# Optimization experiments

Hardware: AMD Instinct MI355X
Metric: run time of the kernel (lower is better)

## Reference

```python
import jax, jax.numpy as jnp
import numpy as np

# ---- constants mirroring the module config ----
TIMESTEPS = 1000
N_GT = 3            # GT phases {stable, pre-shock, shock}
NUM_EXPERTS = 6     # 2 sub-experts per GT phase; phase L -> experts {L, L+3}
LAMBDA_REG = 0.01
LAMBDA_LB = 0.01
PHASE_WEIGHTS = np.array([1.0, 5.0, 5.0], dtype=np.float32)


def _sinusoidal_embed(t, dim):
    # standard DDPM sinusoidal timestep embedding -> [B, dim]
    half = dim // 2
    freqs = jnp.exp(-jnp.log(10000.0) * jnp.arange(half, dtype=jnp.float32) / half)
    args = t.astype(jnp.float32)[:, None] * freqs[None, :]
    return jnp.concatenate([jnp.sin(args), jnp.cos(args)], axis=-1)


def _alphas_bar():
    betas = jnp.linspace(1e-4, 0.02, TIMESTEPS, dtype=jnp.float32)
    return jnp.cumprod(1.0 - betas)


def setup_inputs() -> dict:
    B, Tp, Tf, Df, Ds, dm, E, H = 512, 256, 64, 64, 32, 512, NUM_EXPERTS, 512
    key = jax.random.key(0)
    ks = jax.random.split(key, 16)
    s = 0.02  # init scale
    d_in = Df + 2 * dm  # noisy features + global ctx + t embedding
    return {
        'observed_data': jax.random.normal(ks[0], (B, Tp, Df), jnp.float32),
        'future_data':   jax.random.normal(ks[1], (B, Tf, Df), jnp.float32),
        'static_context': jax.random.normal(ks[2], (B, Ds), jnp.float32),
        'eps':           jax.random.normal(ks[3], (B, Tf, Df), jnp.float32),
        'phase_label':   jax.random.randint(ks[4], (B,), 0, N_GT),
        't':             jax.random.randint(ks[5], (B,), 0, TIMESTEPS),
        'W_enc':    jax.random.normal(ks[6], (Df, dm), jnp.float32) * s,
        'b_enc':    jnp.zeros((dm,), jnp.float32),
        'W_stat':   jax.random.normal(ks[7], (Ds, dm), jnp.float32) * s,
        'W_router': jax.random.normal(ks[8], (dm, E), jnp.float32) * s,
        'b_router': jnp.zeros((E,), jnp.float32),
        'W1': jax.random.normal(ks[9],  (E, d_in, H), jnp.float32) * s,
        'b1': jnp.zeros((E, H), jnp.float32),
        'W2': jax.random.normal(ks[10], (E, H, Df), jnp.float32) * s,
        'b2': jnp.zeros((E, Df), jnp.float32),
    }


def reference(observed_data, future_data, static_context, eps,
              W_enc, b_enc, W_stat, W_router, b_router,
              W1, b1, W2, b2, phase_label, t):
    B, Tf, Df = future_data.shape
    E = W1.shape[0]
    dm = W_enc.shape[1]

    # ---- frozen encoder (torch.no_grad in the original) ----
    ctx_seq = jax.nn.gelu(observed_data @ W_enc + (static_context @ W_stat)[:, None, :] + b_enc)  # [B,Tp,dm]
    global_ctx = ctx_seq.mean(axis=1)                                                             # [B,dm]
    ctx_seq = jax.lax.stop_gradient(ctx_seq)
    global_ctx = jax.lax.stop_gradient(global_ctx)

    # ---- router (trainable) ----
    router_logits = global_ctx @ W_router + b_router        # [B,E]
    router_probs = jax.nn.softmax(router_logits, axis=-1)

    # ---- GT-masked top-1 routing: phase p -> argmax over experts {p, p+3} ----
    selected = jnp.zeros((B,), jnp.int32)
    for p in range(N_GT):
        sub = jnp.stack([router_probs[:, p], router_probs[:, p + N_GT]], axis=1)  # [B,2]
        winner = p + N_GT * jnp.argmax(sub, axis=1).astype(jnp.int32)
        selected = jnp.where(phase_label == p, winner, selected)

    # ---- diffusion scheduler: add_noise ----
    ab = _alphas_bar()[t]                                   # [B]
    noisy_fut = (jnp.sqrt(ab)[:, None, None] * future_data
                 + jnp.sqrt(1.0 - ab)[:, None, None] * eps)  # [B,Tf,Df]

    # ---- expert backbones: run all E experts densely, then gather routed output ----
    t_emb = _sinusoidal_embed(t, dm)                        # [B,dm]
    cond = jnp.concatenate([
        noisy_fut,
        jnp.broadcast_to(global_ctx[:, None, :], (B, Tf, dm)),
        jnp.broadcast_to(t_emb[:, None, :],      (B, Tf, dm)),
    ], axis=-1)                                             # [B,Tf,Din]
    h = jax.nn.gelu(jnp.einsum('btd,edh->ebth', cond, W1) + b1[:, None, None, :])
    outputs_all = jnp.einsum('ebth,ehf->ebtf', h, W2) + b2[:, None, None, :]  # [E,B,Tf,Df]

    pred = outputs_all[selected, jnp.arange(B)]             # [B,Tf,Df] gradient-surgery dispatch
    loss_raw = jnp.mean((pred - eps) ** 2, axis=(1, 2))     # per-sample MSE, [B]

    # weighted_loss * count/B summed over experts == mean(loss_raw * w[selected%3])
    lw = jnp.asarray(PHASE_WEIGHTS)
    w_sample = lw[selected % N_GT]
    total_loss = jnp.mean(loss_raw * w_sample)

    # ---- consistency regularization on a fixed 4-sample subset ----
    S = min(B, 4)
    out_sub = outputs_all[:, :S]                            # [E,S,Tf,Df]
    chain = jnp.float32(0.0)
    for i in [0, 1, 3, 4]:
        if i + 1 < E:
            chain += jnp.mean((out_sub[i] - out_sub[i + 1]) ** 2)
    for i in range(N_GT):
        if i + N_GT < E:
            chain += jnp.mean((out_sub[i] - out_sub[i + N_GT]) ** 2)
    diff = out_sub[:, :, 1:] - out_sub[:, :, :-1]
    smooth = jnp.sum(jnp.mean(diff ** 2, axis=(1, 2, 3)))
    total_loss += (chain + 0.5 * smooth) * LAMBDA_REG

    # ---- load-balance loss ----
    onehot = (selected[:, None] == jnp.arange(E)[None, :]).astype(jnp.float32)  # [B,E]
    f = onehot.mean(axis=0)
    P = router_probs.mean(axis=0)
    total_loss += LAMBDA_LB * E * jnp.sum(f * P)

    return total_loss
```

## Files before the change

kernel.cpp:

```cpp
#include <hip/hip_runtime.h>

typedef float  f32x4 __attribute__((ext_vector_type(4)));
typedef short  s16x8 __attribute__((ext_vector_type(8)));
typedef unsigned short u16;
typedef u16    u16x4 __attribute__((ext_vector_type(4)));

#define TIMESTEPS 1000

#define WS_ALPHAS   0
#define WS_FREQS    1024
#define WS_PROBS    1536
#define WS_SELECTED 4608
#define WS_LOSSB    5632
#define WS_FLAG1    6144
#define WS_PARTS    7680
#define WS_FLAG     7700
#define WS_P0       8192
#define WS_XC       270336
#define WS_HSTAT    532480
#define WS_HSTAT2   794624
#define WS_OUTSUB   806912
#define WS_BIAS     2691072
#define WS_U16BYTE  3620864
#define U_WENCT     0
#define U_W1T       32768
#define U_W2T       3375104

__device__ __forceinline__ u16 f2bf(float x){
    unsigned u = __builtin_bit_cast(unsigned, x);
    unsigned r = (u + 0x7FFFu + ((u >> 16) & 1u)) >> 16;
    return (u16)r;
}

__device__ __forceinline__ float gelu_f(float x){
    float x2 = x * x;
    float t  = x * fmaf(0.035677408136f, x2, 0.7978845608028654f);
    float ex = __builtin_amdgcn_exp2f(t * 2.885390081777927f);
    float r  = __builtin_amdgcn_rcpf(ex + 1.0f);
    return fmaf(-x, r, x);
}

__device__ __forceinline__ void mfma16(f32x4& c, s16x8 a, s16x8 b){
    asm volatile("v_mfma_f32_16x16x32_bf16 %0, %1, %2, %0" : "+v"(c) : "v"(a), "v"(b));
}

__global__ __launch_bounds__(256) void k0(const float* __restrict__ Wenc,
        const float* __restrict__ W1, const float* __restrict__ W2,
        const float* __restrict__ stat, const float* __restrict__ Wstat,
        const float* __restrict__ benc, u16* __restrict__ uws, float* __restrict__ ws){
    __shared__ float sT[64][65];
    float* sp = &sT[0][0];
    int bid = blockIdx.x, tid = threadIdx.x;
    if(bid == 0){
        ws[WS_FREQS + tid] = expf(-logf(10000.0f) * (float)tid / 256.0f);
        float p = 1.f;
        #pragma unroll
        for(int r = 0; r < 4; r++){
            int i = tid*4 + r;
            if(i < TIMESTEPS){
                float beta = 0.0001f + (0.02f - 0.0001f) * ((float)i / 999.0f);
                p *= (1.0f - beta);
            }
        }
        sp[tid] = p;
        __syncthreads();
        for(int st = 1; st < 256; st <<= 1){
            float v = (tid >= st) ? sp[tid - st] : 1.0f;
            __syncthreads();
            sp[tid] *= v;
            __syncthreads();
        }
        float run = (tid == 0) ? 1.0f : sp[tid - 1];
        for(int r = 0; r < 4; r++){
            int i = tid*4 + r;
            if(i < TIMESTEPS){
                float beta = 0.0001f + (0.02f - 0.0001f) * ((float)i / 999.0f);
                run *= (1.0f - beta);
                ws[WS_ALPHAS + i] = run;
            }
        }
        return;
    }
    if(bid <= 8){
        int jt = bid - 1;
        int r = tid >> 2, c0 = (tid & 3) * 16;
        #pragma unroll
        for(int i = 0; i < 4; i++)
            *(f32x4*)&sT[r][c0 + i*4] = *(const f32x4*)&Wenc[(size_t)r*512 + jt*64 + c0 + i*4];
        __syncthreads();
        u16* dst = uws + U_WENCT + (size_t)(jt*64 + r)*64;
        #pragma unroll
        for(int i = 0; i < 4; i++){
            u16x4 pk;
            pk.x = f2bf(sT[c0 + i*4 + 0][r]); pk.y = f2bf(sT[c0 + i*4 + 1][r]);
            pk.z = f2bf(sT[c0 + i*4 + 2][r]); pk.w = f2bf(sT[c0 + i*4 + 3][r]);
            *(u16x4*)&dst[c0 + i*4] = pk;
        }
        return;
    }
    if(bid <= 72){
        float* sSt = sp;
        int g = bid - 9, b0 = g*8;
        sSt[tid] = stat[b0*32 + tid];
        __syncthreads();
        #pragma unroll
        for(int half = 0; half < 2; half++){
            int j = tid + half*256;
            float acc[8] = {0,0,0,0,0,0,0,0};
            for(int s = 0; s < 32; s++){
                float wv = Wstat[s*512 + j];
                #pragma unroll
                for(int bb = 0; bb < 8; bb++) acc[bb] += sSt[bb*32 + s] * wv;
            }
            float bz = benc[j];
            #pragma unroll
            for(int bb = 0; bb < 8; bb++)
                ws[WS_BIAS + (b0 + bb)*512 + j] = acc[bb] + bz;
        }
        return;
    }
    int t = bid - 73;
    const float* src; u16* dst; int K, J, kt, jt;
    if(t < 816){
        int e = t / 136, r = t % 136; kt = r >> 3; jt = r & 7;
        src = W1 + (size_t)e*1088*512; dst = uws + U_W1T + (size_t)e*512*1088; K = 1088; J = 512;
    } else {
        int t2 = t - 816; int e = t2 >> 3; kt = t2 & 7; jt = 0;
        src = W2 + (size_t)e*512*64; dst = uws + U_W2T + (size_t)e*64*512; K = 512; J = 64;
    }
    int r = tid >> 2, c0 = (tid & 3) * 16;
    #pragma unroll
    for(int i = 0; i < 4; i++)
        *(f32x4*)&sT[r][c0 + i*4] = *(const f32x4*)&src[(size_t)(kt*64 + r)*J + jt*64 + c0 + i*4];
    __syncthreads();
    u16* d2 = dst + (size_t)(jt*64 + r)*K + kt*64;
    #pragma unroll
    for(int i = 0; i < 4; i++){
        u16x4 pk;
        pk.x = f2bf(sT[c0 + i*4 + 0][r]); pk.y = f2bf(sT[c0 + i*4 + 1][r]);
        pk.z = f2bf(sT[c0 + i*4 + 2][r]); pk.w = f2bf(sT[c0 + i*4 + 3][r]);
        *(u16x4*)&d2[c0 + i*4] = pk;
    }
}

#define PADX 72
__global__ __launch_bounds__(1024) void k1_enc(const float* __restrict__ obs,
        const u16* __restrict__ uws, const float* __restrict__ Wr,
        const float* __restrict__ br, const int* __restrict__ phase,
        const int* __restrict__ t_arr, float* __restrict__ ws){
    __shared__ u16  sX[256 * PADX];
    __shared__ float sBias[512];
    __shared__ float sG[512];
    __shared__ float sRed[8][6];
    int b = blockIdx.x, tid = threadIdx.x;
    {
        int row = tid >> 2, c0 = (tid & 3) * 16;
        const f32x4* src = (const f32x4*)&obs[((size_t)b*256 + row)*64 + c0];
        u16* dst = &sX[row*PADX + c0];
        #pragma unroll
        for(int i = 0; i < 4; i++){
            f32x4 v = src[i];
            u16x4 pk; pk.x = f2bf(v.x); pk.y = f2bf(v.y); pk.z = f2bf(v.z); pk.w = f2bf(v.w);
            *(u16x4*)(dst + i*4) = pk;
        }
    }
    if(tid < 512) sBias[tid] = ws[WS_BIAS + b*512 + tid];
    __syncthreads();
    int w = tid >> 6, l = tid & 63, lr = l & 15, lk = (l >> 4) * 8;
    const u16* wencT = uws + U_WENCT;
    s16x8 bf[2][2];
    float bias[2];
    #pragma unroll
    for(int n = 0; n < 2; n++){
        int col = w*32 + n*16 + lr;
        bf[n][0] = *(const s16x8*)&wencT[col*64 + lk];
        bf[n][1] = *(const s16x8*)&wencT[col*64 + 32 + lk];
        bias[n]  = sBias[col];
    }
    float cac[2] = {0.f, 0.f};
    for(int mt = 0; mt < 16; mt++){
        s16x8 a0 = *(const s16x8*)&sX[(mt*16 + lr)*PADX + lk];
        s16x8 a1 = *(const s16x8*)&sX[(mt*16 + lr)*PADX + 32 + lk];
        #pragma unroll
        for(int n = 0; n < 2; n++){
            f32x4 acc = {bias[n], bias[n], bias[n], bias[n]};
            mfma16(acc, a0, bf[n][0]);
            mfma16(acc, a1, bf[n][1]);
            cac[n] += gelu_f(acc.x) + gelu_f(acc.y) + gelu_f(acc.z) + gelu_f(acc.w);
        }
    }
    #pragma unroll
    for(int n = 0; n < 2; n++){
        cac[n] += __shfl_xor(cac[n], 16);
        cac[n] += __shfl_xor(cac[n], 32);
    }
    if(l < 16){
        #pragma unroll
        for(int n = 0; n < 2; n++)
            sG[w*32 + n*16 + l] = cac[n] * (1.0f/256.0f);
    }
    __syncthreads();
    if(tid < 512){
        float gv = sG[tid];
        u16* XC = (u16*)(ws + WS_XC);
        XC[b*1024 + tid] = f2bf(gv);
        int tv = t_arr[b];
        float fr = ws[WS_FREQS + (tid & 255)];
        float ang = (float)tv * fr;
        XC[b*1024 + 512 + tid] = f2bf((tid < 256) ? sinf(ang) : cosf(ang));
        float p6[6];
        #pragma unroll
        for(int e = 0; e < 6; e++) p6[e] = gv * Wr[tid*6 + e];
        #pragma unroll
        for(int off = 32; off > 0; off >>= 1)
            #pragma unroll
            for(int e = 0; e < 6; e++) p6[e] += __shfl_down(p6[e], off);
        if(l == 0)
            #pragma unroll
            for(int e = 0; e < 6; e++) sRed[w][e] = p6[e];
    }
    __syncthreads();
    if(tid == 0){
        float logit[6], mx = -1e30f;
        #pragma unroll
        for(int e = 0; e < 6; e++){
            float s = 0.f;
            #pragma unroll
            for(int q = 0; q < 8; q++) s += sRed[q][e];
            logit[e] = s + br[e];
            mx = fmaxf(mx, logit[e]);
        }
        float s = 0.f, p[6];
        #pragma unroll
        for(int e = 0; e < 6; e++){ p[e] = expf(logit[e] - mx); s += p[e]; }
        float inv = 1.0f / s;
        #pragma unroll
        for(int e = 0; e < 6; e++) ws[WS_PROBS + b*6 + e] = p[e] * inv;
        int ph = phase[b];
        int sel = ph + ((logit[ph + 3] > logit[ph]) ? 3 : 0);
        ((int*)ws)[WS_SELECTED + b] = sel;
    }
}

__global__ __launch_bounds__(256) void k3_hstat(const u16* __restrict__ uws,
        const float* __restrict__ b1, float* __restrict__ ws){
    __shared__ int sSrc[64], sDst[64];
    __shared__ int sCnt[8][6], sBase[8][6], sSec[6], sTot[6];
    __shared__ int sChunk[16][3];
    __shared__ int sNch;
    int bid = blockIdx.x, tid = threadIdx.x;
    int w = tid >> 6, l = tid & 63;
    int* wsi = (int*)ws;
    if(bid == 0 && tid == 0) wsi[WS_FLAG] = 0;
    int sv0 = wsi[WS_SELECTED + tid];
    int sv1 = wsi[WS_SELECTED + 256 + tid];
    unsigned long long mym0 = 0, mym1 = 0;
    #pragma unroll
    for(int e = 0; e < 6; e++){
        unsigned long long m0 = __ballot(sv0 == e);
        unsigned long long m1 = __ballot(sv1 == e);
        if(l == 0){ sCnt[w][e] = __popcll(m0); sCnt[4 + w][e] = __popcll(m1); }
        if(sv0 == e) mym0 = m0;
        if(sv1 == e) mym1 = m1;
    }
    if(tid < 64){ sSrc[tid] = 0; sDst[tid] = -1; }
    __syncthreads();
    if(tid == 0){
        int o = 0;
        for(int e = 0; e < 6; e++){
            sSec[e] = o; int t0 = 0;
            for(int g = 0; g < 8; g++){ sBase[g][e] = o; o += sCnt[g][e]; t0 += sCnt[g][e]; }
            sTot[e] = t0; o += 4;
        }
        int nch = 0;
        for(int e = 0; e < 6; e++){
            int len = sTot[e] + 4, st = sSec[e];
            for(int s = 0; s < len; s += 64){
                sChunk[nch][0] = e; sChunk[nch][1] = st + s;
                sChunk[nch][2] = (len - s < 64) ? (len - s) : 64; nch++;
            }
        }
        sNch = nch;
    }
    __syncthreads();
    int c = bid >> 3, jt = bid & 7;
    if(c >= sNch) return;
    int e     = sChunk[c][0];
    int start = sChunk[c][1];
    int len   = sChunk[c][2];
    {
        int rank = __popcll(mym0 & ((1ull << l) - 1ull));
        int pos = sBase[w][sv0] + rank - start;
        if(pos >= 0 && pos < len){ sSrc[pos] = tid; sDst[pos] = WS_HSTAT + tid*512; }
    }
    {
        int rank = __popcll(mym1 & ((1ull << l) - 1ull));
        int pos = sBase[4 + w][sv1] + rank - start;
        if(pos >= 0 && pos < len){ sSrc[pos] = 256 + tid; sDst[pos] = WS_HSTAT + (256 + tid)*512; }
    }
    if(tid < 24){
        int ea = tid >> 2, ba = tid & 3;
        int pos = sSec[ea] + sTot[ea] + ba - start;
        if(pos >= 0 && pos < len){ sSrc[pos] = ba; sDst[pos] = WS_HSTAT2 + (ea*4 + ba)*512; }
    }
    __syncthreads();
    int lr = l & 15, lk = (l >> 4) * 8;
    int col = jt*64 + w*16 + lr;
    const u16* XC = (const u16*)(ws + WS_XC);
    const u16* rowA[4];
    #pragma unroll
    for(int mt = 0; mt < 4; mt++)
        rowA[mt] = XC + (size_t)sSrc[mt*16 + lr]*1024 + lk;
    const u16* bp = uws + U_W1T + ((size_t)e*512 + col)*1088 + 64 + lk;
    f32x4 acc[4];
    {
        float bv = b1[e*512 + col];
        f32x4 z = {bv, bv, bv, bv};
        #pragma unroll
        for(int mt = 0; mt < 4; mt++) acc[mt] = z;
    }
    #pragma unroll 4
    for(int ks = 0; ks < 32; ks++){
        s16x8 bb = *(const s16x8*)(bp + ks*32);
        s16x8 a0 = *(const s16x8*)(rowA[0] + ks*32);
        s16x8 a1 = *(const s16x8*)(rowA[1] + ks*32);
        s16x8 a2 = *(const s16x8*)(rowA[2] + ks*32);
        s16x8 a3 = *(const s16x8*)(rowA[3] + ks*32);
        mfma16(acc[0], a0, bb);
        mfma16(acc[1], a1, bb);
        mfma16(acc[2], a2, bb);
        mfma16(acc[3], a3, bb);
    }
    #pragma unroll
    for(int mt = 0; mt < 4; mt++){
        #pragma unroll
        for(int rg = 0; rg < 4; rg++){
            int r = mt*16 + (l >> 4)*4 + rg;
            int d = sDst[r];
            if(d >= 0) ws[d + col] = acc[mt][rg];
        }
    }
}

#define PADN 72
#define PADH 520
__global__ __launch_bounds__(512) void k4_ffn(const float* __restrict__ fut,
        const float* __restrict__ eps, const int* __restrict__ t_arr,
        const u16* __restrict__ uws, const float* __restrict__ b2,
        float* __restrict__ ws){
    __shared__ u16 sN[64 * PADN];
    __shared__ u16 sH[64 * PADH];
    __shared__ float sHs[512];
    __shared__ float sRed[8];
    int tid = threadIdx.x, bid = blockIdx.x;
    int* wsi = (int*)ws;
    int b, e, store;
    if(bid < 24){ e = bid >> 2; b = bid & 3; store = 1; }
    else { b = bid - 24; e = wsi[WS_SELECTED + b]; store = 0; }
    sHs[tid] = store ? ws[WS_HSTAT2 + (e*4 + b)*512 + tid] : ws[WS_HSTAT + b*512 + tid];
    int tv = t_arr[b];
    float ab = ws[WS_ALPHAS + tv];
    float sa = sqrtf(ab), sb = sqrtf(1.0f - ab);
    {
        int r = tid >> 3, c0 = (tid & 7) * 8;
        const f32x4* pf = (const f32x4*)&fut[((size_t)b*64 + r)*64 + c0];
        const f32x4* pe = (const f32x4*)&eps[((size_t)b*64 + r)*64 + c0];
        f32x4 f0 = pf[0], f1 = pf[1], e0 = pe[0], e1 = pe[1];
        u16x4 p0, p1;
        p0.x = f2bf(sa*f0.x + sb*e0.x); p0.y = f2bf(sa*f0.y + sb*e0.y);
        p0.z = f2bf(sa*f0.z + sb*e0.z); p0.w = f2bf(sa*f0.w + sb*e0.w);
        p1.x = f2bf(sa*f1.x + sb*e1.x); p1.y = f2bf(sa*f1.y + sb*e1.y);
        p1.z = f2bf(sa*f1.z + sb*e1.z); p1.w = f2bf(sa*f1.w + sb*e1.w);
        *(u16x4*)&sN[r*PADN + c0]     = p0;
        *(u16x4*)&sN[r*PADN + c0 + 4] = p1;
    }
    __syncthreads();
    int w = tid >> 6, l = tid & 63, lr = l & 15, lk = (l >> 4) * 8;
    const u16* w1T = uws + U_W1T;
    const u16* w2T = uws + U_W2T;
    s16x8 aw[4][2];
    #pragma unroll
    for(int mt = 0; mt < 4; mt++){
        int jrow = w*64 + mt*16 + lr;
        aw[mt][0] = *(const s16x8*)&w1T[((size_t)e*512 + jrow)*1088 + lk];
        aw[mt][1] = *(const s16x8*)&w1T[((size_t)e*512 + jrow)*1088 + 32 + lk];
    }
    #pragma unroll
    for(int nt = 0; nt < 4; nt++){
        s16x8 nb0 = *(const s16x8*)&sN[(nt*16 + lr)*PADN + lk];
        s16x8 nb1 = *(const s16x8*)&sN[(nt*16 + lr)*PADN + 32 + lk];
        #pragma unroll
        for(int mt = 0; mt < 4; mt++){
            int j0 = w*64 + mt*16 + (l >> 4)*4;
            f32x4 acc = *(const f32x4*)&sHs[j0];
            mfma16(acc, aw[mt][0], nb0);
            mfma16(acc, aw[mt][1], nb1);
            u16x4 pk;
            pk.x = f2bf(gelu_f(acc.x)); pk.y = f2bf(gelu_f(acc.y));
            pk.z = f2bf(gelu_f(acc.z)); pk.w = f2bf(gelu_f(acc.w));
            *(u16x4*)&sH[(nt*16 + lr)*PADH + j0] = pk;
        }
    }
    __syncthreads();
    int mtg = (w >> 2) << 1;
    int nt  = w & 3;
    f32x4 oacc[2];
    {
        float bz = b2[e*64 + nt*16 + lr];
        f32x4 z = {bz, bz, bz, bz}; oacc[0] = z; oacc[1] = z;
    }
    for(int ks = 0; ks < 16; ks++){
        s16x8 bb = *(const s16x8*)&w2T[((size_t)e*64 + nt*16 + lr)*512 + ks*32 + lk];
        #pragma unroll
        for(int i = 0; i < 2; i++){
            s16x8 a = *(const s16x8*)&sH[((mtg + i)*16 + lr)*PADH + ks*32 + lk];
            mfma16(oacc[i], a, bb);
        }
    }
    if(store){
        #pragma unroll
        for(int i = 0; i < 2; i++)
            #pragma unroll
            for(int rg = 0; rg < 4; rg++){
                int row = (mtg + i)*16 + (l >> 4)*4 + rg;
                int col = nt*16 + lr;
                ws[WS_OUTSUB + (e*4 + b)*4096 + row*64 + col] = oacc[i][rg];
            }
    } else {
        float ls = 0.f;
        #pragma unroll
        for(int i = 0; i < 2; i++)
            #pragma unroll
            for(int rg = 0; rg < 4; rg++){
                int row = (mtg + i)*16 + (l >> 4)*4 + rg;
                int col = nt*16 + lr;
                float d = oacc[i][rg] - eps[((size_t)b*64 + row)*64 + col];
                ls += d*d;
            }
        #pragma unroll
        for(int off = 32; off > 0; off >>= 1) ls += __shfl_down(ls, off);
        if(l == 0) sRed[w] = ls;
        __syncthreads();
        if(tid == 0){
            float s = 0.f;
            #pragma unroll
            for(int q = 0; q < 8; q++) s += sRed[q];
            const float pw[3] = {1.f, 5.f, 5.f};
            ws[WS_LOSSB + b] = (s * (1.0f/4096.0f)) * pw[e % 3];
        }
    }
}

__global__ __launch_bounds__(256) void k5_final(float* __restrict__ ws, float* __restrict__ out){
    int bid = blockIdx.x, tid = threadIdx.x;
    int* wsi = (int*)ws;
    if(bid < 13){
        __shared__ float red[256];
        float s = 0.f;
        if(bid < 7){
            const int pa[7] = {0,1,3,4,0,1,2};
            const int pb[7] = {1,2,4,5,3,4,5};
            const float* A  = &ws[WS_OUTSUB + pa[bid]*16384];
            const float* Bp = &ws[WS_OUTSUB + pb[bid]*16384];
            for(int i = tid; i < 4096; i += 256){
                f32x4 a = *(const f32x4*)&A[i*4];
                f32x4 c = *(const f32x4*)&Bp[i*4];
                f32x4 d = a - c;
                s += d.x*d.x + d.y*d.y + d.z*d.z + d.w*d.w;
            }
            s *= (1.0f/16384.0f);
        } else {
            int e = bid - 7;
            const float* O = &ws[WS_OUTSUB + e*16384];
            for(int i = tid; i < 4*63*16; i += 256){
                int sm = i / (63*16); int r = i % (63*16);
                int tf = r / 16; int f4 = (r % 16) * 4;
                f32x4 a = *(const f32x4*)&O[(sm*64 + tf + 1)*64 + f4];
                f32x4 c = *(const f32x4*)&O[(sm*64 + tf)*64 + f4];
                f32x4 d = a - c;
                s += d.x*d.x + d.y*d.y + d.z*d.z + d.w*d.w;
            }
            s *= (1.0f/16128.0f) * 0.5f;
        }
        red[tid] = s;
        __syncthreads();
        for(int st = 128; st > 0; st >>= 1){
            if(tid < st) red[tid] += red[tid + st];
            __syncthreads();
        }
        if(tid == 0){
            ws[WS_PARTS + bid] = red[0];
            __threadfence();
            atomicAdd(&wsi[WS_FLAG], 1);
        }
        return;
    }
    if(tid == 0){
        while(atomicAdd(&wsi[WS_FLAG], 0) < 13) __builtin_amdgcn_s_sleep(2);
    }
    __syncthreads();
    __threadfence();
    __shared__ float sW[4];
    __shared__ float sF[4][6], sP[4][6];
    int w = tid >> 6, l = tid & 63;
    int sel0 = wsi[WS_SELECTED + tid];
    int sel1 = wsi[WS_SELECTED + 256 + tid];
    float lv = ws[WS_LOSSB + tid] + ws[WS_LOSSB + 256 + tid];
    float pv[6], cf[6];
    #pragma unroll
    for(int e = 0; e < 6; e++){
        pv[e] = ws[WS_PROBS + tid*6 + e] + ws[WS_PROBS + (256 + tid)*6 + e];
        cf[e] = ((sel0 == e) ? 1.f : 0.f) + ((sel1 == e) ? 1.f : 0.f);
    }
    #pragma unroll
    for(int off = 32; off > 0; off >>= 1){
        lv += __shfl_down(lv, off);
        #pragma unroll
        for(int e = 0; e < 6; e++){
            pv[e] += __shfl_down(pv[e], off);
            cf[e] += __shfl_down(cf[e], off);
        }
    }
    if(l == 0){
        sW[w] = lv;
        #pragma unroll
        for(int e = 0; e < 6; e++){ sF[w][e] = cf[e]; sP[w][e] = pv[e]; }
    }
    __syncthreads();
    if(tid == 0){
        float total = 0.f;
        for(int q = 0; q < 4; q++) total += sW[q];
        total *= (1.0f/512.0f);
        volatile float* vp = ws + WS_PARTS;
        float reg = 0.f;
        for(int p = 0; p < 13; p++) reg += vp[p];
        total += 0.01f * reg;
        float lb = 0.f;
        for(int e = 0; e < 6; e++){
            float f = 0.f, pp = 0.f;
            for(int q = 0; q < 4; q++){ f += sF[q][e]; pp += sP[q][e]; }
            lb += (f * (1.0f/512.f)) * (pp * (1.0f/512.f));
        }
        out[0] = total + 0.01f * 6.0f * lb;
    }
}

extern "C" void kernel_launch(void* const* d_in, const int* in_sizes, int n_in,
                              void* d_out, int out_size, void* d_ws, size_t ws_size,
                              hipStream_t stream){
    const float* obs  = (const float*)d_in[0];
    const float* fut  = (const float*)d_in[1];
    const float* stat = (const float*)d_in[2];
    const float* eps  = (const float*)d_in[3];
    const int*   phase= (const int*)d_in[4];
    const int*   t    = (const int*)d_in[5];
    const float* Wenc = (const float*)d_in[6];
    const float* benc = (const float*)d_in[7];
    const float* Wstat= (const float*)d_in[8];
    const float* Wr   = (const float*)d_in[9];
    const float* br   = (const float*)d_in[10];
    const float* W1   = (const float*)d_in[11];
    const float* b1   = (const float*)d_in[12];
    const float* W2   = (const float*)d_in[13];
    const float* b2   = (const float*)d_in[14];
    float* ws  = (float*)d_ws;
    u16*   uws = (u16*)((char*)d_ws + WS_U16BYTE);
    float* out = (float*)d_out;

    k0<<<937, 256, 0, stream>>>(Wenc, W1, W2, stat, Wstat, benc, uws, ws);
    k1_enc<<<512, 1024, 0, stream>>>(obs, uws, Wr, br, phase, t, ws);
    k3_hstat<<<112, 256, 0, stream>>>(uws, b1, ws);
    k4_ffn<<<536, 512, 0, stream>>>(fut, eps, t, uws, b2, ws);
    k5_final<<<14, 256, 0, stream>>>(ws, out);
}
```

Measured before the change: 102.5 us.

## Split hidden-stat GEMM along K and FFN along time rows for more blocks

k3_hstat now splits its K reduction into two halves, so it launches twice as many blocks and writes two partial buffers. k4_ffn sums those partials and handles half of the 64 time rows per block, using 256-thread blocks and twice the grid. The consistency-regularisation reduction in k5_final is spread over four times as many blocks, and the per-sample loss weighting moves into the final reduction. The aim is better occupancy of the many CUs on this small-batch workload. The cost is extra partial-sum traffic, W1 slices being reloaded for each time half, and a new workspace buffer placed at the same offset as WS_BIAS.

```diff
diff --git a/kernel.cpp b/kernel.cpp
--- a/kernel.cpp
+++ b/kernel.cpp
@@ -12,15 +12,15 @@
 #define WS_PROBS    1536
 #define WS_SELECTED 4608
 #define WS_LOSSB    5632
-#define WS_FLAG1    6144
 #define WS_PARTS    7680
-#define WS_FLAG     7700
-#define WS_P0       8192
+#define WS_FLAG     7744
+#define WS_HSTATB   8192
 #define WS_XC       270336
 #define WS_HSTAT    532480
 #define WS_HSTAT2   794624
 #define WS_OUTSUB   806912
 #define WS_BIAS     2691072
+#define WS_HSTAT2B  2691072
 #define WS_U16BYTE  3620864
 #define U_WENCT     0
 #define U_W1T       32768
@@ -252,6 +252,7 @@
     int w = tid >> 6, l = tid & 63;
     int* wsi = (int*)ws;
     if(bid == 0 && tid == 0) wsi[WS_FLAG] = 0;
+    int kh = bid & 1, jt = (bid >> 1) & 7, c = bid >> 4;
     int sv0 = wsi[WS_SELECTED + tid];
     int sv1 = wsi[WS_SELECTED + 256 + tid];
     unsigned long long mym0 = 0, mym1 = 0;
@@ -283,25 +284,26 @@
         sNch = nch;
     }
     __syncthreads();
-    int c = bid >> 3, jt = bid & 7;
     if(c >= sNch) return;
     int e     = sChunk[c][0];
     int start = sChunk[c][1];
     int len   = sChunk[c][2];
+    int hstatD  = kh ? WS_HSTATB  : WS_HSTAT;
+    int hstat2D = kh ? WS_HSTAT2B : WS_HSTAT2;
     {
         int rank = __popcll(mym0 & ((1ull << l) - 1ull));
         int pos = sBase[w][sv0] + rank - start;
-        if(pos >= 0 && pos < len){ sSrc[pos] = tid; sDst[pos] = WS_HSTAT + tid*512; }
+        if(pos >= 0 && pos < len){ sSrc[pos] = tid; sDst[pos] = hstatD + tid*512; }
     }
     {
         int rank = __popcll(mym1 & ((1ull << l) - 1ull));
         int pos = sBase[4 + w][sv1] + rank - start;
-        if(pos >= 0 && pos < len){ sSrc[pos] = 256 + tid; sDst[pos] = WS_HSTAT + (256 + tid)*512; }
+        if(pos >= 0 && pos < len){ sSrc[pos] = 256 + tid; sDst[pos] = hstatD + (256 + tid)*512; }
     }
     if(tid < 24){
         int ea = tid >> 2, ba = tid & 3;
         int pos = sSec[ea] + sTot[ea] + ba - start;
-        if(pos >= 0 && pos < len){ sSrc[pos] = ba; sDst[pos] = WS_HSTAT2 + (ea*4 + ba)*512; }
+        if(pos >= 0 && pos < len){ sSrc[pos] = ba; sDst[pos] = hstat2D + (ea*4 + ba)*512; }
     }
     __syncthreads();
     int lr = l & 15, lk = (l >> 4) * 8;
@@ -310,17 +312,17 @@
     const u16* rowA[4];
     #pragma unroll
     for(int mt = 0; mt < 4; mt++)
-        rowA[mt] = XC + (size_t)sSrc[mt*16 + lr]*1024 + lk;
-    const u16* bp = uws + U_W1T + ((size_t)e*512 + col)*1088 + 64 + lk;
+        rowA[mt] = XC + (size_t)sSrc[mt*16 + lr]*1024 + kh*512 + lk;
+    const u16* bp = uws + U_W1T + ((size_t)e*512 + col)*1088 + 64 + kh*512 + lk;
     f32x4 acc[4];
     {
-        float bv = b1[e*512 + col];
+        float bv = kh ? 0.f : b1[e*512 + col];
         f32x4 z = {bv, bv, bv, bv};
         #pragma unroll
         for(int mt = 0; mt < 4; mt++) acc[mt] = z;
     }
     #pragma unroll 4
-    for(int ks = 0; ks < 32; ks++){
+    for(int ks = 0; ks < 16; ks++){
         s16x8 bb = *(const s16x8*)(bp + ks*32);
         s16x8 a0 = *(const s16x8*)(rowA[0] + ks*32);
         s16x8 a1 = *(const s16x8*)(rowA[1] + ks*32);
@@ -344,27 +346,35 @@
 
 #define PADN 72
 #define PADH 520
-__global__ __launch_bounds__(512) void k4_ffn(const float* __restrict__ fut,
+__global__ __launch_bounds__(256) void k4_ffn(const float* __restrict__ fut,
         const float* __restrict__ eps, const int* __restrict__ t_arr,
         const u16* __restrict__ uws, const float* __restrict__ b2,
         float* __restrict__ ws){
-    __shared__ u16 sN[64 * PADN];
-    __shared__ u16 sH[64 * PADH];
+    __shared__ u16 sN[32 * PADN];
+    __shared__ u16 sH[32 * PADH];
     __shared__ float sHs[512];
-    __shared__ float sRed[8];
+    __shared__ float sRed[4];
     int tid = threadIdx.x, bid = blockIdx.x;
     int* wsi = (int*)ws;
-    int b, e, store;
-    if(bid < 24){ e = bid >> 2; b = bid & 3; store = 1; }
-    else { b = bid - 24; e = wsi[WS_SELECTED + b]; store = 0; }
-    sHs[tid] = store ? ws[WS_HSTAT2 + (e*4 + b)*512 + tid] : ws[WS_HSTAT + b*512 + tid];
+    int b, e, store, half;
+    if(bid < 48){ int idx = bid >> 1; half = bid & 1; e = idx >> 2; b = idx & 3; store = 1; }
+    else { int r = bid - 48; b = r >> 1; half = r & 1; e = wsi[WS_SELECTED + b]; store = 0; }
+    int tf0 = half * 32;
+    if(store){
+        int i2 = (e*4 + b)*512;
+        sHs[tid]       = ws[WS_HSTAT2 + i2 + tid]       + ws[WS_HSTAT2B + i2 + tid];
+        sHs[tid + 256] = ws[WS_HSTAT2 + i2 + tid + 256] + ws[WS_HSTAT2B + i2 + tid + 256];
+    } else {
+        sHs[tid]       = ws[WS_HSTAT + b*512 + tid]       + ws[WS_HSTATB + b*512 + tid];
+        sHs[tid + 256] = ws[WS_HSTAT + b*512 + tid + 256] + ws[WS_HSTATB + b*512 + tid + 256];
+    }
     int tv = t_arr[b];
     float ab = ws[WS_ALPHAS + tv];
     float sa = sqrtf(ab), sb = sqrtf(1.0f - ab);
     {
         int r = tid >> 3, c0 = (tid & 7) * 8;
-        const f32x4* pf = (const f32x4*)&fut[((size_t)b*64 + r)*64 + c0];
-        const f32x4* pe = (const f32x4*)&eps[((size_t)b*64 + r)*64 + c0];
+        const f32x4* pf = (const f32x4*)&fut[((size_t)b*64 + tf0 + r)*64 + c0];
+        const f32x4* pe = (const f32x4*)&eps[((size_t)b*64 + tf0 + r)*64 + c0];
         f32x4 f0 = pf[0], f1 = pf[1], e0 = pe[0], e1 = pe[1];
         u16x4 p0, p1;
         p0.x = f2bf(sa*f0.x + sb*e0.x); p0.y = f2bf(sa*f0.y + sb*e0.y);
@@ -378,23 +388,24 @@
     int w = tid >> 6, l = tid & 63, lr = l & 15, lk = (l >> 4) * 8;
     const u16* w1T = uws + U_W1T;
     const u16* w2T = uws + U_W2T;
-    s16x8 aw[4][2];
-    #pragma unroll
-    for(int mt = 0; mt < 4; mt++){
-        int jrow = w*64 + mt*16 + lr;
-        aw[mt][0] = *(const s16x8*)&w1T[((size_t)e*512 + jrow)*1088 + lk];
-        aw[mt][1] = *(const s16x8*)&w1T[((size_t)e*512 + jrow)*1088 + 32 + lk];
-    }
-    #pragma unroll
-    for(int nt = 0; nt < 4; nt++){
-        s16x8 nb0 = *(const s16x8*)&sN[(nt*16 + lr)*PADN + lk];
-        s16x8 nb1 = *(const s16x8*)&sN[(nt*16 + lr)*PADN + 32 + lk];
-        #pragma unroll
-        for(int mt = 0; mt < 4; mt++){
-            int j0 = w*64 + mt*16 + (l >> 4)*4;
-            f32x4 acc = *(const f32x4*)&sHs[j0];
-            mfma16(acc, aw[mt][0], nb0);
-            mfma16(acc, aw[mt][1], nb1);
+    s16x8 nb[2][2];
+    #pragma unroll
+    for(int nt = 0; nt < 2; nt++){
+        nb[nt][0] = *(const s16x8*)&sN[(nt*16 + lr)*PADN + lk];
+        nb[nt][1] = *(const s16x8*)&sN[(nt*16 + lr)*PADN + 32 + lk];
+    }
+    #pragma unroll
+    for(int mt = 0; mt < 8; mt++){
+        int jrow = w*128 + mt*16 + lr;
+        s16x8 aw0 = *(const s16x8*)&w1T[((size_t)e*512 + jrow)*1088 + lk];
+        s16x8 aw1 = *(const s16x8*)&w1T[((size_t)e*512 + jrow)*1088 + 32 + lk];
+        int j0 = w*128 + mt*16 + (l >> 4)*4;
+        f32x4 hsv = *(const f32x4*)&sHs[j0];
+        #pragma unroll
+        for(int nt = 0; nt < 2; nt++){
+            f32x4 acc = hsv;
+            mfma16(acc, aw0, nb[nt][0]);
+            mfma16(acc, aw1, nb[nt][1]);
             u16x4 pk;
             pk.x = f2bf(gelu_f(acc.x)); pk.y = f2bf(gelu_f(acc.y));
             pk.z = f2bf(gelu_f(acc.z)); pk.w = f2bf(gelu_f(acc.w));
@@ -402,18 +413,17 @@
         }
     }
     __syncthreads();
-    int mtg = (w >> 2) << 1;
-    int nt  = w & 3;
+    int nt_o = w;
     f32x4 oacc[2];
     {
-        float bz = b2[e*64 + nt*16 + lr];
+        float bz = b2[e*64 + nt_o*16 + lr];
         f32x4 z = {bz, bz, bz, bz}; oacc[0] = z; oacc[1] = z;
     }
     for(int ks = 0; ks < 16; ks++){
-        s16x8 bb = *(const s16x8*)&w2T[((size_t)e*64 + nt*16 + lr)*512 + ks*32 + lk];
+        s16x8 bb = *(const s16x8*)&w2T[((size_t)e*64 + nt_o*16 + lr)*512 + ks*32 + lk];
         #pragma unroll
         for(int i = 0; i < 2; i++){
-            s16x8 a = *(const s16x8*)&sH[((mtg + i)*16 + lr)*PADH + ks*32 + lk];
+            s16x8 a = *(const s16x8*)&sH[(i*16 + lr)*PADH + ks*32 + lk];
             mfma16(oacc[i], a, bb);
         }
     }
@@ -422,8 +432,8 @@
         for(int i = 0; i < 2; i++)
             #pragma unroll
             for(int rg = 0; rg < 4; rg++){
-                int row = (mtg + i)*16 + (l >> 4)*4 + rg;
-                int col = nt*16 + lr;
+                int row = tf0 + i*16 + (l >> 4)*4 + rg;
+                int col = nt_o*16 + lr;
                 ws[WS_OUTSUB + (e*4 + b)*4096 + row*64 + col] = oacc[i][rg];
             }
     } else {
@@ -432,8 +442,8 @@
         for(int i = 0; i < 2; i++)
             #pragma unroll
             for(int rg = 0; rg < 4; rg++){
-                int row = (mtg + i)*16 + (l >> 4)*4 + rg;
-                int col = nt*16 + lr;
+                int row = tf0 + i*16 + (l >> 4)*4 + rg;
+                int col = nt_o*16 + lr;
                 float d = oacc[i][rg] - eps[((size_t)b*64 + row)*64 + col];
                 ls += d*d;
             }
@@ -442,11 +452,8 @@
         if(l == 0) sRed[w] = ls;
         __syncthreads();
         if(tid == 0){
-            float s = 0.f;
-            #pragma unroll
-            for(int q = 0; q < 8; q++) s += sRed[q];
-            const float pw[3] = {1.f, 5.f, 5.f};
-            ws[WS_LOSSB + b] = (s * (1.0f/4096.0f)) * pw[e % 3];
+            float s = sRed[0] + sRed[1] + sRed[2] + sRed[3];
+            ws[WS_LOSSB + half*512 + b] = s;
         }
     }
 }
@@ -454,15 +461,16 @@
 __global__ __launch_bounds__(256) void k5_final(float* __restrict__ ws, float* __restrict__ out){
     int bid = blockIdx.x, tid = threadIdx.x;
     int* wsi = (int*)ws;
-    if(bid < 13){
+    if(bid < 52){
         __shared__ float red[256];
+        int part = bid >> 2, q = bid & 3;
         float s = 0.f;
-        if(bid < 7){
+        if(part < 7){
             const int pa[7] = {0,1,3,4,0,1,2};
             const int pb[7] = {1,2,4,5,3,4,5};
-            const float* A  = &ws[WS_OUTSUB + pa[bid]*16384];
-            const float* Bp = &ws[WS_OUTSUB + pb[bid]*16384];
-            for(int i = tid; i < 4096; i += 256){
+            const float* A  = &ws[WS_OUTSUB + pa[part]*16384];
+            const float* Bp = &ws[WS_OUTSUB + pb[part]*16384];
+            for(int i = q*1024 + tid; i < q*1024 + 1024; i += 256){
                 f32x4 a = *(const f32x4*)&A[i*4];
                 f32x4 c = *(const f32x4*)&Bp[i*4];
                 f32x4 d = a - c;
@@ -470,9 +478,9 @@
             }
             s *= (1.0f/16384.0f);
         } else {
-            int e = bid - 7;
+            int e = part - 7;
             const float* O = &ws[WS_OUTSUB + e*16384];
-            for(int i = tid; i < 4*63*16; i += 256){
+            for(int i = q*1008 + tid; i < q*1008 + 1008; i += 256){
                 int sm = i / (63*16); int r = i % (63*16);
                 int tf = r / 16; int f4 = (r % 16) * 4;
                 f32x4 a = *(const f32x4*)&O[(sm*64 + tf + 1)*64 + f4];
@@ -496,7 +504,7 @@
         return;
     }
     if(tid == 0){
-        while(atomicAdd(&wsi[WS_FLAG], 0) < 13) __builtin_amdgcn_s_sleep(2);
+        while(atomicAdd(&wsi[WS_FLAG], 0) < 52) __builtin_amdgcn_s_sleep(2);
     }
     __syncthreads();
     __threadfence();
@@ -505,7 +513,10 @@
     int w = tid >> 6, l = tid & 63;
     int sel0 = wsi[WS_SELECTED + tid];
     int sel1 = wsi[WS_SELECTED + 256 + tid];
-    float lv = ws[WS_LOSSB + tid] + ws[WS_LOSSB + 256 + tid];
+    float wg0 = (sel0 % 3 == 0) ? 1.f : 5.f;
+    float wg1 = (sel1 % 3 == 0) ? 1.f : 5.f;
+    float lv = (ws[WS_LOSSB + tid] + ws[WS_LOSSB + 512 + tid]) * (1.0f/4096.0f) * wg0
+             + (ws[WS_LOSSB + 256 + tid] + ws[WS_LOSSB + 768 + tid]) * (1.0f/4096.0f) * wg1;
     float pv[6], cf[6];
     #pragma unroll
     for(int e = 0; e < 6; e++){
@@ -533,7 +544,7 @@
         total *= (1.0f/512.0f);
         volatile float* vp = ws + WS_PARTS;
         float reg = 0.f;
-        for(int p = 0; p < 13; p++) reg += vp[p];
+        for(int p = 0; p < 52; p++) reg += vp[p];
         total += 0.01f * reg;
         float lb = 0.f;
         for(int e = 0; e < 6; e++){
@@ -569,7 +580,7 @@
 
     k0<<<937, 256, 0, stream>>>(Wenc, W1, W2, stat, Wstat, benc, uws, ws);
     k1_enc<<<512, 1024, 0, stream>>>(obs, uws, Wr, br, phase, t, ws);
-    k3_hstat<<<112, 256, 0, stream>>>(uws, b1, ws);
-    k4_ffn<<<536, 512, 0, stream>>>(fut, eps, t, uws, b2, ws);
-    k5_final<<<14, 256, 0, stream>>>(ws, out);
-}
+    k3_hstat<<<224, 256, 0, stream>>>(uws, b1, ws);
+    k4_ffn<<<1072, 256, 0, stream>>>(fut, eps, t, uws, b2, ws);
+    k5_final<<<53, 256, 0, stream>>>(ws, out);
+}
```

Result: faster. 95.48 us (-6.9%).
